# Kernel optimization log

Hardware: AMD Instinct MI355X
Metric: run time of the kernel (lower is better)

The kernel has to match this reference:

```python
import jax, jax.numpy as jnp
import numpy as np

TAU = 2.0  # LIF membrane time constant (tau=2.0)
V_TH = 1.0  # spiking threshold (spikingjelly default)

@jax.custom_vjp
def spike(v):
    # Heaviside spike at v >= 0 (input is v - V_TH)
    return (v >= 0.0).astype(v.dtype)

def _spike_fwd(v):
    return spike(v), v

def _spike_bwd(v, g):
    # ATan surrogate gradient (spikingjelly default, alpha=2):
    # d/dv = alpha / (2 * (1 + (pi/2 * alpha * v)^2)) = 1 / (1 + (pi*v)^2)
    return (g / (1.0 + (jnp.pi * v) ** 2),)

spike.defvjp(_spike_fwd, _spike_bwd)

def lif_linear(x, w):
    """SpikLinearLayer: Linear (no bias) then multi-step LIF over leading T axis.
    x: [T, B, N, Din], w: [Dout, Din] -> spikes [T, B, N, Dout]
    LIF: v <- v + (y - v)/tau ; s = H(v - vth) ; hard reset v <- v*(1-s)
    """
    y = jnp.einsum('tbnd,ed->tbne', x, w)
    def step(v, yt):
        v = v + (yt - v) / TAU
        s = spike(v - V_TH)
        return v * (1.0 - s), s
    _, spikes = jax.lax.scan(step, jnp.zeros_like(y[0]), y)
    return spikes

def setup_inputs() -> dict:
    key = jax.random.key(0)
    k0, k1, k2, k3 = jax.random.split(key, 4)
    T, B, N, D, L = 4, 32, 1024, 256, 2
    x = jax.random.normal(k0, (T, B, N, D), dtype=jnp.float32)
    w_in = jax.random.normal(k1, (2 * D, D), dtype=jnp.float32) * 0.05
    w_hidden = jax.random.normal(k2, (L, 2 * D, 2 * D), dtype=jnp.float32) * 0.05
    w_out = jax.random.normal(k3, (D, 2 * D), dtype=jnp.float32) * 0.05
    return {"x": x, "w_in": w_in, "w_hidden": w_hidden, "w_out": w_out}

def reference(x, w_in, w_hidden, w_out):
    # TemporalBlock.forward
    h = lif_linear(x, w_in)                       # [T,B,N,2D]
    for l in range(w_hidden.shape[0]):
        h = h * (1.0 - lif_linear(h, w_hidden[l]))  # multiplicative spike gate
    return lif_linear(h, w_out)                   # [T,B,N,D]
```

## Files before the change

### kernel.cpp

```cpp
#include <hip/hip_runtime.h>
#include <stdint.h>

typedef __attribute__((ext_vector_type(8))) short short8;
typedef __attribute__((ext_vector_type(4))) float f32x4;

constexpr int T_ = 4;
constexpr int BNTOT = 32768;

__device__ __forceinline__ uint32_t bf1(float f) {
    uint32_t x = __builtin_bit_cast(uint32_t, f);
    return (x + 0x7FFFu + ((x >> 16) & 1u)) >> 16;
}
__device__ __forceinline__ uint32_t pk(float lo, float hi) {
    return bf1(lo) | (bf1(hi) << 16);
}

__device__ __forceinline__ short8 expand8(uint2 r) {
    uint4 o;
    o.x = __builtin_amdgcn_perm(0u, r.x, 0x0C010C00u) * 0x3F80u;
    o.y = __builtin_amdgcn_perm(0u, r.x, 0x0C030C02u) * 0x3F80u;
    o.z = __builtin_amdgcn_perm(0u, r.y, 0x0C010C00u) * 0x3F80u;
    o.w = __builtin_amdgcn_perm(0u, r.y, 0x0C030C02u) * 0x3F80u;
    return __builtin_bit_cast(short8, o);
}

__global__ __launch_bounds__(256)
void cvt_tiled(const float* __restrict__ in, ushort* __restrict__ out) {
    const int g  = blockIdx.x * 256 + threadIdx.x;
    const int kg = g & 31;
    const int r  = (g >> 5) & 15;
    const int bt = g >> 9;
    const float* src = in + ((size_t)(bt * 16 + r)) * 256 + kg * 8;
    const float4 a = *(const float4*)src;
    const float4 b = *(const float4*)(src + 4);
    uint4 o;
    o.x = pk(a.x, a.y); o.y = pk(a.z, a.w);
    o.z = pk(b.x, b.y); o.w = pk(b.z, b.w);
    *(uint4*)(out + ((size_t)(bt * 32 + kg)) * 128 + r * 8) = o;
}

template <int MODE, int K, int NOUT>
__global__ __launch_bounds__(256, 2)
void lif_mfma(const void* __restrict__ Av,
              const float* __restrict__ W,
              void* __restrict__ Out)
{
    constexpr int NS = K / 32;
    constexpr int KG = K / 8;
    constexpr int NCOLT = NOUT / 64;
    __shared__ __align__(16) char smem[NS * 4096];

    const int tid = threadIdx.x;
    const int l   = tid & 63;
    const int w   = tid >> 6;

    const int id  = blockIdx.x;
    const int xcd = id & 7;
    const int j_  = id >> 3;
    const int row0 = (xcd * 64 + j_ / NCOLT) * 64;
    const int col0 = (j_ % NCOLT) * 64;

    {
        constexpr int ITERS = 64 * KG / 256;
#pragma unroll
        for (int i = 0; i < ITERS; ++i) {
            const int idx = i * 256 + tid;
            const int c   = idx / KG;
            const int kg  = idx % KG;
            const float* wp = W + (size_t)(col0 + c) * K + kg * 8;
            const float4 f0 = *(const float4*)wp;
            const float4 f1 = *(const float4*)(wp + 4);
            uint4 o;
            o.x = pk(f0.x, f0.y); o.y = pk(f0.z, f0.w);
            o.z = pk(f1.x, f1.y); o.w = pk(f1.z, f1.w);
            const int s = kg >> 2, g = kg & 3;
            *(uint4*)(smem + ((c >> 4) * NS + s) * 1024 + (c & 15) * 64 +
                      ((g ^ ((c >> 1) & 3)) * 16)) = o;
        }
    }
    __syncthreads();

    const char* bbase = smem + (l & 15) * 64 + (((l >> 4) ^ ((l >> 1) & 3)) * 16);
    const int rb = (row0 >> 4) + w;

    f32x4 acc[T_][4];
#pragma unroll
    for (int t = 0; t < T_; ++t)
#pragma unroll
        for (int n = 0; n < 4; ++n) acc[t][n] = (f32x4)0.f;

    size_t aunit[T_];
#pragma unroll
    for (int t = 0; t < T_; ++t)
        aunit[t] = ((size_t)(t * (BNTOT / 16) + rb)) * KG + (l >> 4);

    auto loadAb = [&](int s, short8 a[T_]) {
#pragma unroll
        for (int t = 0; t < T_; ++t)
            a[t] = *(const short8*)((const ushort*)Av +
                     (aunit[t] + s * 4) * 128 + (l & 15) * 8);
    };
    auto loadAu = [&](int s, uint2 a[T_]) {
#pragma unroll
        for (int t = 0; t < T_; ++t)
            a[t] = *(const uint2*)((const uint8_t*)Av +
                     (aunit[t] + s * 4) * 128 + (l & 15) * 8);
    };
    auto stepB = [&](const short8 a[T_], int s) {
        short8 bfr[4];
#pragma unroll
        for (int n = 0; n < 4; ++n)
            bfr[n] = *(const short8*)(bbase + (n * NS + s) * 1024);
#pragma unroll
        for (int t = 0; t < T_; ++t)
#pragma unroll
            for (int n = 0; n < 4; ++n)
                acc[t][n] = __builtin_amdgcn_mfma_f32_16x16x32_bf16(
                    a[t], bfr[n], acc[t][n], 0, 0, 0);
    };
    auto stepU = [&](const uint2 a[T_], int s) {
        short8 bfr[4];
#pragma unroll
        for (int n = 0; n < 4; ++n)
            bfr[n] = *(const short8*)(bbase + (n * NS + s) * 1024);
#pragma unroll
        for (int t = 0; t < T_; ++t) {
            const short8 af = expand8(a[t]);
#pragma unroll
            for (int n = 0; n < 4; ++n)
                acc[t][n] = __builtin_amdgcn_mfma_f32_16x16x32_bf16(
                    af, bfr[n], acc[t][n], 0, 0, 0);
        }
    };

    if constexpr (MODE == 0) {
        short8 a0[T_], a1[T_];
        loadAb(0, a0);
        for (int s = 0; s < NS; s += 2) {
            loadAb(s + 1, a1);
            stepB(a0, s);
            loadAb(s + 2 < NS ? s + 2 : 0, a0);
            stepB(a1, s + 1);
        }
    } else {
        uint2 a0[T_], a1[T_];
        loadAu(0, a0);
        for (int s = 0; s < NS; s += 2) {
            loadAu(s + 1, a1);
            stepU(a0, s);
            loadAu(s + 2 < NS ? s + 2 : 0, a0);
            stepU(a1, s + 1);
        }
    }

#pragma unroll
    for (int n = 0; n < 4; ++n) {
#pragma unroll
        for (int j = 0; j < 4; ++j) {
            const int rl   = (l >> 4) * 4 + j;
            const int grow = row0 + w * 16 + rl;
            const int c    = col0 + n * 16 + (l & 15);
            float v = 0.f;
#pragma unroll
            for (int t = 0; t < T_; ++t) {
                v = 0.5f * (v + acc[t][n][j]);
                const bool sp = (v >= 1.f);
                if (sp) v = 0.f;
                if constexpr (MODE == 2) {
                    ((float*)Out)[((size_t)(t * BNTOT + grow)) * NOUT + c] =
                        sp ? 1.f : 0.f;
                } else {
                    const size_t tb =
                        ((size_t)(t * (BNTOT / 16) + (grow >> 4)) * (NOUT / 8) +
                         (c >> 3)) * 128 + rl * 8 + (c & 7);
                    if constexpr (MODE == 0) {
                        ((uint8_t*)Out)[tb] = sp ? 1 : 0;
                    } else {
                        const uint8_t h = ((const uint8_t*)Av)[tb];
                        ((uint8_t*)Out)[tb] = sp ? 0 : h;
                    }
                }
            }
        }
    }
}

extern "C" void kernel_launch(void* const* d_in, const int* in_sizes, int n_in,
                              void* d_out, int out_size, void* d_ws, size_t ws_size,
                              hipStream_t stream)
{
    const float* x     = (const float*)d_in[0];
    const float* w_in  = (const float*)d_in[1];
    const float* w_h   = (const float*)d_in[2];
    const float* w_out = (const float*)d_in[3];

    ushort*  xbf = (ushort*)d_out;
    uint8_t* hA  = (uint8_t*)d_ws;
    uint8_t* hB  = hA + (size_t)T_ * BNTOT * 512;
    float*   out = (float*)d_out;

    cvt_tiled<<<16384, 256, 0, stream>>>(x, xbf);

    lif_mfma<0, 256, 512><<<4096, 256, 0, stream>>>(xbf, w_in, hA);
    lif_mfma<1, 512, 512><<<4096, 256, 0, stream>>>(hA, w_h, hB);
    lif_mfma<1, 512, 512><<<4096, 256, 0, stream>>>(hB, w_h + 512 * 512, hA);
    lif_mfma<2, 512, 256><<<2048, 256, 0, stream>>>(hA, w_out, out);
}
```

Baseline: 348.7 us.

## Fuse input bf16 conversion into GEMM, panel weights in LDS, stage epilogue stores

Drops the separate fp32-to-bf16 conversion kernel. The first layer now reads fp32 x directly and packs it to bf16 in registers. Weights are staged into LDS in 8-step K panels, which shrinks shared memory to 32KB and allows occupancy of 4 blocks per SM instead of 2. The A prefetch is deepened to four buffers. Epilogues write spikes through LDS and emit coalesced 16-byte global stores, using a byte mask AND for the gating layers. The costs are extra barriers between panels, more live registers, and uncoalesced-style fp32 loads of x in the first layer.

```diff
diff --git a/kernel.cpp b/kernel.cpp
--- a/kernel.cpp
+++ b/kernel.cpp
@@ -24,31 +24,17 @@
     return __builtin_bit_cast(short8, o);
 }
 
-__global__ __launch_bounds__(256)
-void cvt_tiled(const float* __restrict__ in, ushort* __restrict__ out) {
-    const int g  = blockIdx.x * 256 + threadIdx.x;
-    const int kg = g & 31;
-    const int r  = (g >> 5) & 15;
-    const int bt = g >> 9;
-    const float* src = in + ((size_t)(bt * 16 + r)) * 256 + kg * 8;
-    const float4 a = *(const float4*)src;
-    const float4 b = *(const float4*)(src + 4);
-    uint4 o;
-    o.x = pk(a.x, a.y); o.y = pk(a.z, a.w);
-    o.z = pk(b.x, b.y); o.w = pk(b.z, b.w);
-    *(uint4*)(out + ((size_t)(bt * 32 + kg)) * 128 + r * 8) = o;
-}
-
 template <int MODE, int K, int NOUT>
-__global__ __launch_bounds__(256, 2)
+__global__ __launch_bounds__(256, 4)
 void lif_mfma(const void* __restrict__ Av,
               const float* __restrict__ W,
               void* __restrict__ Out)
 {
     constexpr int NS = K / 32;
-    constexpr int KG = K / 8;
+    constexpr int PANEL = (NS > 8) ? 8 : NS;
+    constexpr int HALVES = NS / PANEL;
     constexpr int NCOLT = NOUT / 64;
-    __shared__ __align__(16) char smem[NS * 4096];
+    __shared__ __align__(16) char smem[32768];
 
     const int tid = threadIdx.x;
     const int l   = tid & 63;
@@ -60,28 +46,23 @@
     const int row0 = (xcd * 64 + j_ / NCOLT) * 64;
     const int col0 = (j_ % NCOLT) * 64;
 
-    {
-        constexpr int ITERS = 64 * KG / 256;
-#pragma unroll
-        for (int i = 0; i < ITERS; ++i) {
+    const char* bbase = smem + (l & 15) * 64 + (((l >> 4) ^ ((l >> 1) & 3)) * 16);
+
+    auto stageB = [&](int hf) {
+#pragma unroll
+        for (int i = 0; i < 8; ++i) {
             const int idx = i * 256 + tid;
-            const int c   = idx / KG;
-            const int kg  = idx % KG;
-            const float* wp = W + (size_t)(col0 + c) * K + kg * 8;
+            const int c = idx >> 5, kgl = idx & 31;
+            const float* wp = W + (size_t)(col0 + c) * K + (hf * PANEL * 4 + kgl) * 8;
             const float4 f0 = *(const float4*)wp;
             const float4 f1 = *(const float4*)(wp + 4);
             uint4 o;
             o.x = pk(f0.x, f0.y); o.y = pk(f0.z, f0.w);
             o.z = pk(f1.x, f1.y); o.w = pk(f1.z, f1.w);
-            const int s = kg >> 2, g = kg & 3;
-            *(uint4*)(smem + ((c >> 4) * NS + s) * 1024 + (c & 15) * 64 +
-                      ((g ^ ((c >> 1) & 3)) * 16)) = o;
-        }
-    }
-    __syncthreads();
-
-    const char* bbase = smem + (l & 15) * 64 + (((l >> 4) ^ ((l >> 1) & 3)) * 16);
-    const int rb = (row0 >> 4) + w;
+            *(uint4*)(smem + ((c >> 4) * PANEL + (kgl >> 2)) * 1024 + (c & 15) * 64 +
+                      (((kgl & 3) ^ ((c >> 1) & 3)) * 16)) = o;
+        }
+    };
 
     f32x4 acc[T_][4];
 #pragma unroll
@@ -89,28 +70,34 @@
 #pragma unroll
         for (int n = 0; n < 4; ++n) acc[t][n] = (f32x4)0.f;
 
-    size_t aunit[T_];
-#pragma unroll
-    for (int t = 0; t < T_; ++t)
-        aunit[t] = ((size_t)(t * (BNTOT / 16) + rb)) * KG + (l >> 4);
-
-    auto loadAb = [&](int s, short8 a[T_]) {
+    const uint8_t* au_base = (const uint8_t*)Av +
+        (((size_t)((row0 >> 4) + w)) * (K / 8) + (l >> 4)) * 128 + (l & 15) * 8;
+    const float* ax_base = (const float*)Av +
+        ((size_t)(row0 + w * 16 + (l & 15))) * K + (l >> 4) * 8;
+
+    auto loadAu = [&](int s, uint2 a[T_]) {
 #pragma unroll
         for (int t = 0; t < T_; ++t)
-            a[t] = *(const short8*)((const ushort*)Av +
-                     (aunit[t] + s * 4) * 128 + (l & 15) * 8);
-    };
-    auto loadAu = [&](int s, uint2 a[T_]) {
-#pragma unroll
-        for (int t = 0; t < T_; ++t)
-            a[t] = *(const uint2*)((const uint8_t*)Av +
-                     (aunit[t] + s * 4) * 128 + (l & 15) * 8);
-    };
-    auto stepB = [&](const short8 a[T_], int s) {
+            a[t] = *(const uint2*)(au_base +
+                     ((size_t)t * (BNTOT / 16) * (K / 8) + s * 4) * 128);
+    };
+    auto loadAx = [&](int s, short8 a[T_]) {
+#pragma unroll
+        for (int t = 0; t < T_; ++t) {
+            const float* p = ax_base + (size_t)t * BNTOT * K + s * 32;
+            const float4 u = *(const float4*)p;
+            const float4 v2 = *(const float4*)(p + 4);
+            uint4 o;
+            o.x = pk(u.x, u.y);  o.y = pk(u.z, u.w);
+            o.z = pk(v2.x, v2.y); o.w = pk(v2.z, v2.w);
+            a[t] = __builtin_bit_cast(short8, o);
+        }
+    };
+    auto stepF = [&](const short8 a[T_], int sl) {
         short8 bfr[4];
 #pragma unroll
         for (int n = 0; n < 4; ++n)
-            bfr[n] = *(const short8*)(bbase + (n * NS + s) * 1024);
+            bfr[n] = *(const short8*)(bbase + (n * PANEL + sl) * 1024);
 #pragma unroll
         for (int t = 0; t < T_; ++t)
 #pragma unroll
@@ -118,11 +105,11 @@
                 acc[t][n] = __builtin_amdgcn_mfma_f32_16x16x32_bf16(
                     a[t], bfr[n], acc[t][n], 0, 0, 0);
     };
-    auto stepU = [&](const uint2 a[T_], int s) {
+    auto stepU = [&](const uint2 a[T_], int sl) {
         short8 bfr[4];
 #pragma unroll
         for (int n = 0; n < 4; ++n)
-            bfr[n] = *(const short8*)(bbase + (n * NS + s) * 1024);
+            bfr[n] = *(const short8*)(bbase + (n * PANEL + sl) * 1024);
 #pragma unroll
         for (int t = 0; t < T_; ++t) {
             const short8 af = expand8(a[t]);
@@ -133,54 +120,102 @@
         }
     };
 
+    stageB(0);
+    __syncthreads();
+
     if constexpr (MODE == 0) {
-        short8 a0[T_], a1[T_];
-        loadAb(0, a0);
+        short8 aA[T_], aB[T_];
+        loadAx(0, aA);
         for (int s = 0; s < NS; s += 2) {
-            loadAb(s + 1, a1);
-            stepB(a0, s);
-            loadAb(s + 2 < NS ? s + 2 : 0, a0);
-            stepB(a1, s + 1);
+            loadAx(s + 1 < NS ? s + 1 : 0, aB);
+            stepF(aA, s);
+            loadAx(s + 2 < NS ? s + 2 : 0, aA);
+            stepF(aB, s + 1);
         }
     } else {
-        uint2 a0[T_], a1[T_];
-        loadAu(0, a0);
-        for (int s = 0; s < NS; s += 2) {
-            loadAu(s + 1, a1);
-            stepU(a0, s);
-            loadAu(s + 2 < NS ? s + 2 : 0, a0);
-            stepU(a1, s + 1);
+        uint2 aA[T_], aB[T_], aC[T_], aD[T_];
+        loadAu(0, aA);
+        loadAu(1, aB);
+        for (int hf = 0; hf < HALVES; ++hf) {
+            if (hf) { __syncthreads(); stageB(hf); __syncthreads(); }
+            const int base = hf * PANEL;
+#pragma unroll
+            for (int ss = 0; ss < PANEL; ss += 4) {
+                const int s = base + ss;
+                loadAu(s + 2 < NS ? s + 2 : 0, aC); stepU(aA, ss + 0);
+                loadAu(s + 3 < NS ? s + 3 : 0, aD); stepU(aB, ss + 1);
+                loadAu(s + 4 < NS ? s + 4 : 0, aA); stepU(aC, ss + 2);
+                loadAu(s + 5 < NS ? s + 5 : 0, aB); stepU(aD, ss + 3);
+            }
         }
     }
 
-#pragma unroll
-    for (int n = 0; n < 4; ++n) {
-#pragma unroll
-        for (int j = 0; j < 4; ++j) {
-            const int rl   = (l >> 4) * 4 + j;
-            const int grow = row0 + w * 16 + rl;
-            const int c    = col0 + n * 16 + (l & 15);
-            float v = 0.f;
-#pragma unroll
-            for (int t = 0; t < T_; ++t) {
-                v = 0.5f * (v + acc[t][n][j]);
-                const bool sp = (v >= 1.f);
-                if (sp) v = 0.f;
-                if constexpr (MODE == 2) {
-                    ((float*)Out)[((size_t)(t * BNTOT + grow)) * NOUT + c] =
+    __syncthreads();
+
+    if constexpr (MODE == 2) {
+        float* fl = (float*)smem;
+        float v[4][4];
+#pragma unroll
+        for (int n = 0; n < 4; ++n)
+#pragma unroll
+            for (int j = 0; j < 4; ++j) v[n][j] = 0.f;
+#pragma unroll
+        for (int t = 0; t < T_; ++t) {
+#pragma unroll
+            for (int n = 0; n < 4; ++n)
+#pragma unroll
+                for (int j = 0; j < 4; ++j) {
+                    v[n][j] = 0.5f * (v[n][j] + acc[t][n][j]);
+                    const bool sp = (v[n][j] >= 1.f);
+                    if (sp) v[n][j] = 0.f;
+                    fl[(w * 16 + (l >> 4) * 4 + j) * 68 + n * 16 + (l & 15)] =
                         sp ? 1.f : 0.f;
-                } else {
-                    const size_t tb =
-                        ((size_t)(t * (BNTOT / 16) + (grow >> 4)) * (NOUT / 8) +
-                         (c >> 3)) * 128 + rl * 8 + (c & 7);
-                    if constexpr (MODE == 0) {
-                        ((uint8_t*)Out)[tb] = sp ? 1 : 0;
-                    } else {
-                        const uint8_t h = ((const uint8_t*)Av)[tb];
-                        ((uint8_t*)Out)[tb] = sp ? 0 : h;
-                    }
                 }
+            __syncthreads();
+            const int r  = tid >> 2;
+            const int cb = (tid & 3) * 16;
+            float* op = (float*)Out +
+                ((size_t)(t * BNTOT + row0 + r)) * NOUT + col0 + cb;
+#pragma unroll
+            for (int k = 0; k < 4; ++k)
+                *(float4*)(op + k * 4) = *(const float4*)&fl[r * 68 + cb + k * 4];
+            __syncthreads();
+        }
+    } else {
+        char* el = smem;
+        float v[4][4];
+#pragma unroll
+        for (int n = 0; n < 4; ++n)
+#pragma unroll
+            for (int j = 0; j < 4; ++j) v[n][j] = 0.f;
+#pragma unroll
+        for (int t = 0; t < T_; ++t)
+#pragma unroll
+            for (int n = 0; n < 4; ++n)
+#pragma unroll
+                for (int j = 0; j < 4; ++j) {
+                    v[n][j] = 0.5f * (v[n][j] + acc[t][n][j]);
+                    const bool sp = (v[n][j] >= 1.f);
+                    if (sp) v[n][j] = 0.f;
+                    el[t * 4096 + w * 1024 + (n * 2 + ((l & 15) >> 3)) * 128 +
+                       ((l >> 4) * 4 + j) * 8 + (l & 7)] =
+                        (MODE == 0) ? (sp ? 1 : 0) : (sp ? 0 : 0xFF);
+                }
+        __syncthreads();
+        const int lin = tid * 64;
+        const int t  = lin >> 12;
+        const int w2 = (lin >> 10) & 3;
+        const int cg = (lin >> 7) & 7;
+        const size_t gb = ((size_t)(t * (BNTOT / 16) + (row0 >> 4) + w2) *
+                          (NOUT / 8) + (col0 >> 3) + cg) * 128 + (lin & 127);
+#pragma unroll
+        for (int k = 0; k < 4; ++k) {
+            uint4 m = *(const uint4*)(el + lin + k * 16);
+            if constexpr (MODE == 1) {
+                const uint4 h = *(const uint4*)((const uint8_t*)Av + gb + k * 16);
+                m.x &= h.x; m.y &= h.y; m.z &= h.z; m.w &= h.w;
             }
+            *(uint4*)((uint8_t*)Out + gb + k * 16) = m;
         }
     }
 }
@@ -194,14 +229,11 @@
     const float* w_h   = (const float*)d_in[2];
     const float* w_out = (const float*)d_in[3];
 
-    ushort*  xbf = (ushort*)d_out;
     uint8_t* hA  = (uint8_t*)d_ws;
     uint8_t* hB  = hA + (size_t)T_ * BNTOT * 512;
     float*   out = (float*)d_out;
 
-    cvt_tiled<<<16384, 256, 0, stream>>>(x, xbf);
-
-    lif_mfma<0, 256, 512><<<4096, 256, 0, stream>>>(xbf, w_in, hA);
+    lif_mfma<0, 256, 512><<<4096, 256, 0, stream>>>(x, w_in, hA);
     lif_mfma<1, 512, 512><<<4096, 256, 0, stream>>>(hA, w_h, hB);
     lif_mfma<1, 512, 512><<<4096, 256, 0, stream>>>(hB, w_h + 512 * 512, hA);
     lif_mfma<2, 512, 256><<<2048, 256, 0, stream>>>(hA, w_out, out);
```

Result: slower. 522.3 us (+49.8%).
